# Kernel optimization log

Hardware: AMD Instinct MI355X
Metric: run time of the kernel (lower is better)

The kernel has to match this reference:

```python
import jax, jax.numpy as jnp
import numpy as np

H = 8
D_MODEL = 512
D_K = D_MODEL // H
NEG = -1e9


def setup_inputs() -> dict:
    key = jax.random.key(0)
    ks = jax.random.split(key, 11)
    B, S = 2, 2048
    scale = 1.0 / np.sqrt(D_MODEL)
    inp = {
        'query': jax.random.normal(ks[0], (B, S, D_MODEL), dtype=jnp.float32),
        'key': jax.random.normal(ks[1], (B, S, D_MODEL), dtype=jnp.float32),
        'value': jax.random.normal(ks[2], (B, S, D_MODEL), dtype=jnp.float32),
        'Wq': jax.random.normal(ks[3], (D_MODEL, D_MODEL), dtype=jnp.float32) * scale,
        'bq': jnp.zeros((D_MODEL,), dtype=jnp.float32),
        'Wk': jax.random.normal(ks[4], (D_MODEL, D_MODEL), dtype=jnp.float32) * scale,
        'bk': jnp.zeros((D_MODEL,), dtype=jnp.float32),
        'Wv': jax.random.normal(ks[5], (D_MODEL, D_MODEL), dtype=jnp.float32) * scale,
        'bv': jnp.zeros((D_MODEL,), dtype=jnp.float32),
        'Wo': jax.random.normal(ks[6], (D_MODEL, D_MODEL), dtype=jnp.float32) * scale,
        'bo': jnp.zeros((D_MODEL,), dtype=jnp.float32),
    }
    return inp


def reference(query, key, value, Wq, bq, Wk, bk, Wv, bv, Wo, bo):
    B, S, _ = query.shape
    # QKV projections (nn.Linear: x @ W.T + b), split into heads -> [B, H, S, D_K]
    def proj(x, W, b):
        return (x @ W.T + b).reshape(B, S, H, D_K).transpose(0, 2, 1, 3)

    q = proj(query, Wq, bq)
    k = proj(key, Wk, bk)
    v = proj(value, Wv, bv)

    scores = jnp.einsum('bhqd,bhkd->bhqk', q, k) / jnp.sqrt(jnp.float32(D_K))
    # diagonal mask (mask=True): token cannot attend to itself
    diag = jnp.eye(S, dtype=bool)
    scores = jnp.where(diag, NEG, scores)

    p_attn = jax.nn.softmax(scores, axis=-1)  # [B, H, S, S]
    x = jnp.einsum('bhqk,bhkd->bhqd', p_attn, v)
    x = x.transpose(0, 2, 1, 3).reshape(B, S, H * D_K)
    return x @ Wo.T + bo
```

## Files before the change

kernel.cpp:

```cpp
#include <hip/hip_runtime.h>
#include <hip/hip_bf16.h>
#include <hip/hip_fp16.h>
#include <math.h>

#define NUM_H 8
#define DK    64
#define DM    512
#define SEQ   2048
#define NB    2
#define MROWS (NB*SEQ)
#define NZ    4

typedef unsigned short u16;
typedef unsigned int   u32;
typedef __attribute__((ext_vector_type(8))) __bf16 bf16x8;
typedef __attribute__((ext_vector_type(4))) short  s16x4;
typedef __attribute__((ext_vector_type(4))) float  f32x4;

__device__ __forceinline__ u16 f2bf(float v) {
    union { __bf16 h; u16 u; } x; x.h = (__bf16)v; return x.u;
}
__device__ __forceinline__ u16 f2h(float v) {
    union { _Float16 h; u16 u; } x; x.h = (_Float16)v; return x.u;
}
__device__ __forceinline__ bf16x8 ld_bf8(const u16* p) {
    union { uint4 u; bf16x8 v; } t;
    t.u = *(const uint4*)p;
    return t.v;
}
__device__ __forceinline__ uint4 pack8bf(const float* f) {
    uint4 o;
    o.x = (u32)f2bf(f[0]) | ((u32)f2bf(f[1]) << 16);
    o.y = (u32)f2bf(f[2]) | ((u32)f2bf(f[3]) << 16);
    o.z = (u32)f2bf(f[4]) | ((u32)f2bf(f[5]) << 16);
    o.w = (u32)f2bf(f[6]) | ((u32)f2bf(f[7]) << 16);
    return o;
}
__device__ __forceinline__ float fexp2(float x) {
#if defined(__has_builtin) && __has_builtin(__builtin_amdgcn_exp2f)
    return __builtin_amdgcn_exp2f(x);
#else
    return exp2f(x);
#endif
}

__device__ __forceinline__ f32x4 mfma16bf(s16x4 a, s16x4 b, f32x4 c) {
#if defined(__has_builtin) && __has_builtin(__builtin_amdgcn_mfma_f32_16x16x16bf16_1k)
    return __builtin_amdgcn_mfma_f32_16x16x16bf16_1k(a, b, c, 0, 0, 0);
#else
    asm("v_mfma_f32_16x16x16_bf16 %0, %1, %2, %0" : "+v"(c) : "v"(a), "v"(b));
    return c;
#endif
}

__global__ __launch_bounds__(256) void convW(
    const float* __restrict__ Wq, const float* __restrict__ Wk,
    const float* __restrict__ Wv, const float* __restrict__ Wo,
    u16* __restrict__ Wscr)
{
    const int z = blockIdx.y;
    const float* src = (z == 0) ? Wq : (z == 1) ? Wk : (z == 2) ? Wv : Wo;
    u16* dst = Wscr + (size_t)z * 262144;
    int i = (blockIdx.x * 256 + threadIdx.x) * 8;
    float4 a = *(const float4*)(src + i);
    float4 b = *(const float4*)(src + i + 4);
    float f[8] = {a.x, a.y, a.z, a.w, b.x, b.y, b.z, b.w};
    *(uint4*)&dst[i] = pack8bf(f);
}

#define MODE_QK 0
#define MODE_VT 1
#define MODE_FIN 2

template<int MODE>
__device__ __forceinline__ void gemm_core(
    const void* __restrict__ Xv, const u16* __restrict__ Wb,
    const float* __restrict__ bias, const float* __restrict__ ClP,
    void* __restrict__ outv,
    u16* As, u16* Bs, int row0, int col0)
{
    const int tid = threadIdx.x;
    const int lane = tid & 63, w = tid >> 6;
    const int ln15 = lane & 15, quad = lane >> 4;
    const int wm = (w >> 1) * 32, wn = (w & 1) * 32;

    int cb0 = 0, cs0 = 0, cb1 = 0, cs1 = 0;
    if (MODE == MODE_FIN) {
        int m0 = row0 + (tid >> 3), m1 = m0 + 32;
        cb0 = (m0 >> 11) * NUM_H; cs0 = m0 & (SEQ - 1);
        cb1 = (m1 >> 11) * NUM_H; cs1 = m1 & (SEQ - 1);
    }

    f32x4 acc[2][2];
#pragma unroll
    for (int mt = 0; mt < 2; ++mt)
#pragma unroll
        for (int nt = 0; nt < 2; ++nt) acc[mt][nt] = (f32x4){0.f, 0.f, 0.f, 0.f};

    for (int kt = 0; kt < DM; kt += 64) {
        __syncthreads();
        if (MODE == MODE_FIN) {
            const int h = kt >> 6;
            float l0 = ClP[(cb0 + h) * SEQ + cs0] + ClP[32768 + (cb0 + h) * SEQ + cs0]
                     + ClP[65536 + (cb0 + h) * SEQ + cs0] + ClP[98304 + (cb0 + h) * SEQ + cs0];
            float l1 = ClP[(cb1 + h) * SEQ + cs1] + ClP[32768 + (cb1 + h) * SEQ + cs1]
                     + ClP[65536 + (cb1 + h) * SEQ + cs1] + ClP[98304 + (cb1 + h) * SEQ + cs1];
            float scr[2] = {64.f / l0, 64.f / l1};
#pragma unroll
            for (int g = 0; g < 2; ++g) {
                int r = g * 32 + (tid >> 3);
                int c = (tid & 7) * 8;
                const u16* pp = (const u16*)Xv + (size_t)(row0 + r) * DM + kt + c;
                union { uint4 u; __half2 h2[4]; } u0, u1, u2, u3;
                u0.u = *(const uint4*)pp;
                u1.u = *(const uint4*)(pp + 2097152);
                u2.u = *(const uint4*)(pp + 2 * 2097152);
                u3.u = *(const uint4*)(pp + 3 * 2097152);
                float f[8];
                float sc = scr[g];
#pragma unroll
                for (int j = 0; j < 4; ++j) {
                    __half2 s2 = __hadd2(__hadd2(u0.h2[j], u1.h2[j]),
                                         __hadd2(u2.h2[j], u3.h2[j]));
                    float2 fl = __half22float2(s2);
                    f[2 * j]     = fl.x * sc;
                    f[2 * j + 1] = fl.y * sc;
                }
                *(uint4*)&As[r * 72 + c] = pack8bf(f);
            }
        } else {
#pragma unroll
            for (int g = 0; g < 2; ++g) {
                int idx = g * 2048 + tid * 8;
                int r = idx >> 6, c = idx & 63;
                const float* xp = (const float*)Xv + (size_t)(row0 + r) * DM + kt + c;
                float4 a = *(const float4*)xp;
                float4 b2 = *(const float4*)(xp + 4);
                float f[8] = {a.x, a.y, a.z, a.w, b2.x, b2.y, b2.z, b2.w};
                *(uint4*)&As[r * 72 + c] = pack8bf(f);
            }
        }
#pragma unroll
        for (int g = 0; g < 2; ++g) {
            int idx = g * 2048 + tid * 8;
            int r = idx >> 6, c = idx & 63;
            *(uint4*)&Bs[r * 72 + c] =
                *(const uint4*)(Wb + (size_t)(col0 + r) * DM + kt + c);
        }
        __syncthreads();

#pragma unroll
        for (int ks = 0; ks < 2; ++ks) {
            bf16x8 af[2], bfr[2];
#pragma unroll
            for (int mt = 0; mt < 2; ++mt)
                af[mt] = ld_bf8(&As[(wm + mt * 16 + ln15) * 72 + ks * 32 + quad * 8]);
#pragma unroll
            for (int nt = 0; nt < 2; ++nt)
                bfr[nt] = ld_bf8(&Bs[(wn + nt * 16 + ln15) * 72 + ks * 32 + quad * 8]);
#pragma unroll
            for (int mt = 0; mt < 2; ++mt)
#pragma unroll
                for (int nt = 0; nt < 2; ++nt)
                    acc[mt][nt] = __builtin_amdgcn_mfma_f32_16x16x32_bf16(
                        af[mt], bfr[nt], acc[mt][nt], 0, 0, 0);
        }
    }

    float bc[2];
#pragma unroll
    for (int nt = 0; nt < 2; ++nt) bc[nt] = bias[col0 + wn + nt * 16 + ln15];
    const int h = col0 >> 6;

    if (MODE == MODE_FIN) {
        float* outF = (float*)outv;
#pragma unroll
        for (int mt = 0; mt < 2; ++mt)
#pragma unroll
            for (int r = 0; r < 4; ++r) {
                int m = row0 + wm + mt * 16 + quad * 4 + r;
#pragma unroll
                for (int nt = 0; nt < 2; ++nt)
                    outF[(size_t)m * DM + col0 + wn + nt * 16 + ln15] = acc[mt][nt][r] + bc[nt];
            }
    } else if (MODE == MODE_QK) {
        u16* outB = (u16*)outv;
#pragma unroll
        for (int mt = 0; mt < 2; ++mt)
#pragma unroll
            for (int r = 0; r < 4; ++r) {
                int m = row0 + wm + mt * 16 + quad * 4 + r;
                int b = m >> 11, s2 = m & (SEQ - 1);
#pragma unroll
                for (int nt = 0; nt < 2; ++nt) {
                    int dk = wn + nt * 16 + ln15;
                    outB[((size_t)((b * NUM_H + h) * SEQ + s2)) * DK + dk] =
                        f2bf(acc[mt][nt][r] + bc[nt]);
                }
            }
    } else {
        u16* outB = (u16*)outv;
        __syncthreads();
#pragma unroll
        for (int mt = 0; mt < 2; ++mt)
#pragma unroll
            for (int nt = 0; nt < 2; ++nt) {
                int dk = wn + nt * 16 + ln15;
#pragma unroll
                for (int r = 0; r < 4; ++r) {
                    int sl = wm + mt * 16 + quad * 4 + r;
                    As[dk * 72 + sl] = f2bf(acc[mt][nt][r] + bc[nt]);
                }
            }
        __syncthreads();
        int dk = tid >> 2, ch = (tid & 3) * 16;
        int b = row0 >> 11, s0 = row0 & (SEQ - 1);
        size_t base = ((size_t)((b * NUM_H + h) * DK + dk)) * SEQ + s0 + ch;
        *(uint4*)&outB[base]     = *(const uint4*)&As[dk * 72 + ch];
        *(uint4*)&outB[base + 8] = *(const uint4*)&As[dk * 72 + ch + 8];
    }
}

__global__ __launch_bounds__(256) void qkv_mfma(
    const float* __restrict__ xq, const float* __restrict__ xk, const float* __restrict__ xv,
    const u16* __restrict__ Wscr,
    const float* __restrict__ b0, const float* __restrict__ b1, const float* __restrict__ b2,
    u16* __restrict__ oQ, u16* __restrict__ oK, u16* __restrict__ oVt)
{
    __shared__ u16 As[64 * 72];
    __shared__ u16 Bs[64 * 72];
    const int row0 = blockIdx.x * 64, col0 = blockIdx.y * 64;
    const int z = blockIdx.z;
    const u16* W = Wscr + (size_t)z * 262144;
    if (z == 2)
        gemm_core<MODE_VT>(xv, W, b2, nullptr, oVt, As, Bs, row0, col0);
    else if (z == 0)
        gemm_core<MODE_QK>(xq, W, b0, nullptr, oQ, As, Bs, row0, col0);
    else
        gemm_core<MODE_QK>(xk, W, b1, nullptr, oK, As, Bs, row0, col0);
}

__global__ __launch_bounds__(256) void final_mfma(
    const u16* __restrict__ Pd, const u16* __restrict__ Wbf,
    const float* __restrict__ Cl, const float* __restrict__ bias,
    float* __restrict__ out)
{
    __shared__ u16 As[64 * 72];
    __shared__ u16 Bs[64 * 72];
    gemm_core<MODE_FIN>(Pd, Wbf, bias, Cl, out, As, Bs,
                        blockIdx.x * 64, blockIdx.y * 64);
}

#define LSTR 72
#define SCL2  0.18033688f
#define BIA2 -5.7708020f
__global__ __launch_bounds__(256) void attn_mfma(
    const u16* __restrict__ Qg, const u16* __restrict__ Kg,
    const u16* __restrict__ Vtg, u16* __restrict__ Pd, float* __restrict__ Cl)
{
    __shared__ u16 Klds[64 * LSTR];
    __shared__ u16 Vtlds[64 * LSTR];

    const int tid = threadIdx.x;
    const int lane = tid & 63;
    const int w = tid >> 6;
    const int ln15 = lane & 15;
    const int quad = lane >> 4;
    const int bh = blockIdx.y;
    const int b = bh >> 3, h = bh & 7;
    const int qb = blockIdx.x * 64;
    const int z = blockIdx.z;
    const int k0 = z * (SEQ / NZ), k1 = k0 + SEQ / NZ;

    const u16* Qp = Qg + (size_t)bh * SEQ * DK;
    const u16* Kp = Kg + (size_t)bh * SEQ * DK;
    const u16* Vp = Vtg + (size_t)bh * DK * SEQ;

    const int myq = w * 16 + ln15;
    const int qrow = qb + myq;
    const bf16x8 qa0 = ld_bf8(&Qp[(size_t)qrow * DK + quad * 8]);
    const bf16x8 qa1 = ld_bf8(&Qp[(size_t)qrow * DK + 32 + quad * 8]);

    const bool mrow = (quad == (ln15 >> 2));
    const int  mr   = ln15 & 3;

    const s16x4 onesb = (s16x4){(short)0x3F80, (short)0x3F80,
                                (short)0x3F80, (short)0x3F80};

    f32x4 O[4];
    f32x4 Lacc = (f32x4){0.f, 0.f, 0.f, 0.f};
#pragma unroll
    for (int nt = 0; nt < 4; ++nt) O[nt] = (f32x4){0.f, 0.f, 0.f, 0.f};

    const int sr = tid >> 3;
    const int scl = (tid & 7) * 8;
    const u16* kp0 = &Kp[(size_t)sr * DK + scl];
    const u16* kp1 = &Kp[(size_t)(sr + 32) * DK + scl];
    const u16* vp0 = &Vp[(size_t)sr * SEQ + scl];
    const u16* vp1 = &Vp[(size_t)(sr + 32) * SEQ + scl];

    uint4 kreg0 = *(const uint4*)&kp0[(size_t)k0 * DK];
    uint4 kreg1 = *(const uint4*)&kp1[(size_t)k0 * DK];
    uint4 vreg0 = *(const uint4*)&vp0[k0];
    uint4 vreg1 = *(const uint4*)&vp1[k0];

    for (int kt = k0; kt < k1; kt += 64) {
        *(uint4*)&Klds[sr * LSTR + scl]         = kreg0;
        *(uint4*)&Klds[(sr + 32) * LSTR + scl]  = kreg1;
        *(uint4*)&Vtlds[sr * LSTR + scl]        = vreg0;
        *(uint4*)&Vtlds[(sr + 32) * LSTR + scl] = vreg1;
        __syncthreads();

        if (kt + 64 < k1) {
            kreg0 = *(const uint4*)&kp0[(size_t)(kt + 64) * DK];
            kreg1 = *(const uint4*)&kp1[(size_t)(kt + 64) * DK];
            vreg0 = *(const uint4*)&vp0[kt + 64];
            vreg1 = *(const uint4*)&vp1[kt + 64];
        }

        const bool diagt = (kt == qb);
        s16x4 pa[4];
#pragma unroll
        for (int nt2 = 0; nt2 < 4; ++nt2) {
            bf16x8 kb0 = ld_bf8(&Klds[(nt2 * 16 + ln15) * LSTR + quad * 8]);
            bf16x8 kb1 = ld_bf8(&Klds[(nt2 * 16 + ln15) * LSTR + 32 + quad * 8]);
            f32x4 zacc = (f32x4){0.f, 0.f, 0.f, 0.f};
            zacc = __builtin_amdgcn_mfma_f32_16x16x32_bf16(kb0, qa0, zacc, 0, 0, 0);
            zacc = __builtin_amdgcn_mfma_f32_16x16x32_bf16(kb1, qa1, zacc, 0, 0, 0);
            union { u16 u[4]; s16x4 v; } pk;
#pragma unroll
            for (int r = 0; r < 4; ++r)
                pk.u[r] = f2bf(fexp2(fmaf(zacc[r], SCL2, BIA2)));
            if (diagt && nt2 == w) {
#pragma unroll
                for (int r = 0; r < 4; ++r)
                    if (mrow && r == mr) pk.u[r] = 0;
            }
            pa[nt2] = pk.v;
        }

        const u16* vb_base = &Vtlds[ln15 * LSTR + quad * 4];
        __builtin_amdgcn_s_setprio(1);
#pragma unroll
        for (int nt2 = 0; nt2 < 4; ++nt2)
            Lacc = mfma16bf(pa[nt2], onesb, Lacc);
#pragma unroll
        for (int nt = 0; nt < 4; ++nt) {
#pragma unroll
            for (int nt2 = 0; nt2 < 4; ++nt2) {
                s16x4 vb = *(const s16x4*)&vb_base[nt * 16 * LSTR + nt2 * 16];
                O[nt] = mfma16bf(pa[nt2], vb, O[nt]);
            }
        }
        __builtin_amdgcn_s_setprio(0);
        __syncthreads();
    }

    if (ln15 == 0) {
#pragma unroll
        for (int r = 0; r < 4; ++r)
            Cl[(size_t)z * 32768 + bh * SEQ + qb + w * 16 + quad * 4 + r] = Lacc[r];
    }

#pragma unroll
    for (int r = 0; r < 4; ++r) {
        int s = qb + w * 16 + quad * 4 + r;
        size_t base = (size_t)z * 2097152 + ((size_t)(b * SEQ + s)) * DM + h * DK;
#pragma unroll
        for (int nt = 0; nt < 4; ++nt)
            Pd[base + nt * 16 + ln15] = f2h(O[nt][r] * 0.015625f);
    }
}

extern "C" void kernel_launch(void* const* d_in, const int* in_sizes, int n_in,
                              void* d_out, int out_size, void* d_ws, size_t ws_size,
                              hipStream_t stream) {
    const float* q  = (const float*)d_in[0];
    const float* k  = (const float*)d_in[1];
    const float* v  = (const float*)d_in[2];
    const float* Wq = (const float*)d_in[3];
    const float* bq = (const float*)d_in[4];
    const float* Wk = (const float*)d_in[5];
    const float* bk = (const float*)d_in[6];
    const float* Wv = (const float*)d_in[7];
    const float* bv = (const float*)d_in[8];
    const float* Wo = (const float*)d_in[9];
    const float* bo = (const float*)d_in[10];
    float* out = (float*)d_out;

    const size_t TSZ = (size_t)MROWS * DM;
    u16* Qb   = (u16*)d_ws;
    u16* Kb   = Qb + TSZ;
    u16* Vtb  = Qb + 2 * TSZ;
    float* Cl = (float*)(Qb + 3 * TSZ);
    u16* Wscr = (u16*)(Cl + 131072);
    u16* Pd   = Wscr + 4 * 262144;

    dim3 blk(256);
    hipLaunchKernelGGL(convW, dim3(128, 4), blk, 0, stream, Wq, Wk, Wv, Wo, Wscr);
    dim3 gq(MROWS / 64, DM / 64, 3);
    hipLaunchKernelGGL(qkv_mfma, gq, blk, 0, stream,
                       q, k, v, Wscr, bq, bk, bv, Qb, Kb, Vtb);
    dim3 ga(SEQ / 64, NB * NUM_H, NZ);
    hipLaunchKernelGGL(attn_mfma, ga, blk, 0, stream, Qb, Kb, Vtb, Pd, Cl);
    dim3 gf(MROWS / 64, DM / 64);
    hipLaunchKernelGGL(final_mfma, gf, blk, 0, stream, Pd, Wscr + 3 * 262144, Cl, bo, out);
}
```

Baseline: 149.9 us.

## Pre-convert activations to bf16 and register-prefetch next GEMM tile

The weight-conversion kernel is extended to also convert the three fp32 input activations to bf16 in a workspace buffer, so the QKV GEMM loads half as many bytes per tile. The GEMM core is restructured to prefetch the next K-tile into registers while MFMAs run on the current shared tile. The final GEMM precomputes all per-head softmax normalizers up front instead of per iteration. This adds an extra full pass over the inputs (read fp32, write bf16, reread) plus register pressure from eight prefetched uint4 in FIN mode.

```diff
diff --git a/kernel.cpp b/kernel.cpp
--- a/kernel.cpp
+++ b/kernel.cpp
@@ -53,14 +53,24 @@
 #endif
 }
 
-__global__ __launch_bounds__(256) void convW(
+__global__ __launch_bounds__(256) void convAll(
     const float* __restrict__ Wq, const float* __restrict__ Wk,
     const float* __restrict__ Wv, const float* __restrict__ Wo,
-    u16* __restrict__ Wscr)
+    const float* __restrict__ xq, const float* __restrict__ xk,
+    const float* __restrict__ xv,
+    u16* __restrict__ Wscr, u16* __restrict__ Xb)
 {
     const int z = blockIdx.y;
-    const float* src = (z == 0) ? Wq : (z == 1) ? Wk : (z == 2) ? Wv : Wo;
-    u16* dst = Wscr + (size_t)z * 262144;
+    const float* src;
+    u16* dst;
+    if (z < 4) {
+        if (blockIdx.x >= 128) return;
+        src = (z == 0) ? Wq : (z == 1) ? Wk : (z == 2) ? Wv : Wo;
+        dst = Wscr + (size_t)z * 262144;
+    } else {
+        src = (z == 4) ? xq : (z == 5) ? xk : xv;
+        dst = Xb + (size_t)(z - 4) * 2097152;
+    }
     int i = (blockIdx.x * 256 + threadIdx.x) * 8;
     float4 a = *(const float4*)(src + i);
     float4 b = *(const float4*)(src + i + 4);
@@ -74,7 +84,7 @@
 
 template<int MODE>
 __device__ __forceinline__ void gemm_core(
-    const void* __restrict__ Xv, const u16* __restrict__ Wb,
+    const u16* __restrict__ Xb, const u16* __restrict__ Wb,
     const float* __restrict__ bias, const float* __restrict__ ClP,
     void* __restrict__ outv,
     u16* As, u16* Bs, int row0, int col0)
@@ -83,12 +93,30 @@
     const int lane = tid & 63, w = tid >> 6;
     const int ln15 = lane & 15, quad = lane >> 4;
     const int wm = (w >> 1) * 32, wn = (w & 1) * 32;
-
-    int cb0 = 0, cs0 = 0, cb1 = 0, cs1 = 0;
+    const int sr = tid >> 3;
+    const int scl = (tid & 7) * 8;
+
+    const u16* a0p = Xb + (size_t)(row0 + sr) * DM + scl;
+    const u16* a1p = Xb + (size_t)(row0 + 32 + sr) * DM + scl;
+    const u16* b0p = Wb + (size_t)(col0 + sr) * DM + scl;
+    const u16* b1p = Wb + (size_t)(col0 + 32 + sr) * DM + scl;
+
+    float scr0[8], scr1[8];
     if (MODE == MODE_FIN) {
-        int m0 = row0 + (tid >> 3), m1 = m0 + 32;
-        cb0 = (m0 >> 11) * NUM_H; cs0 = m0 & (SEQ - 1);
-        cb1 = (m1 >> 11) * NUM_H; cs1 = m1 & (SEQ - 1);
+        int m0 = row0 + sr, m1 = m0 + 32;
+        int cb0 = (m0 >> 11) * NUM_H, cs0 = m0 & (SEQ - 1);
+        int cb1 = (m1 >> 11) * NUM_H, cs1 = m1 & (SEQ - 1);
+#pragma unroll
+        for (int hh = 0; hh < 8; ++hh) {
+            float l0 = 0.f, l1 = 0.f;
+#pragma unroll
+            for (int zz = 0; zz < NZ; ++zz) {
+                l0 += ClP[zz * 32768 + (cb0 + hh) * SEQ + cs0];
+                l1 += ClP[zz * 32768 + (cb1 + hh) * SEQ + cs1];
+            }
+            scr0[hh] = 64.f / l0;
+            scr1[hh] = 64.f / l1;
+        }
     }
 
     f32x4 acc[2][2];
@@ -97,57 +125,75 @@
 #pragma unroll
         for (int nt = 0; nt < 2; ++nt) acc[mt][nt] = (f32x4){0.f, 0.f, 0.f, 0.f};
 
+    uint4 ra0, ra1, rb0, rb1;
+    uint4 rp00, rp01, rp02, rp03, rp10, rp11, rp12, rp13;
+    if (MODE == MODE_FIN) {
+        rp00 = *(const uint4*)(a0p);
+        rp01 = *(const uint4*)(a0p + 2097152);
+        rp02 = *(const uint4*)(a0p + 2 * 2097152);
+        rp03 = *(const uint4*)(a0p + 3 * 2097152);
+        rp10 = *(const uint4*)(a1p);
+        rp11 = *(const uint4*)(a1p + 2097152);
+        rp12 = *(const uint4*)(a1p + 2 * 2097152);
+        rp13 = *(const uint4*)(a1p + 3 * 2097152);
+    } else {
+        ra0 = *(const uint4*)a0p;
+        ra1 = *(const uint4*)a1p;
+    }
+    rb0 = *(const uint4*)b0p;
+    rb1 = *(const uint4*)b1p;
+
+#pragma unroll
     for (int kt = 0; kt < DM; kt += 64) {
-        __syncthreads();
+        const int h = kt >> 6;
         if (MODE == MODE_FIN) {
-            const int h = kt >> 6;
-            float l0 = ClP[(cb0 + h) * SEQ + cs0] + ClP[32768 + (cb0 + h) * SEQ + cs0]
-                     + ClP[65536 + (cb0 + h) * SEQ + cs0] + ClP[98304 + (cb0 + h) * SEQ + cs0];
-            float l1 = ClP[(cb1 + h) * SEQ + cs1] + ClP[32768 + (cb1 + h) * SEQ + cs1]
-                     + ClP[65536 + (cb1 + h) * SEQ + cs1] + ClP[98304 + (cb1 + h) * SEQ + cs1];
-            float scr[2] = {64.f / l0, 64.f / l1};
-#pragma unroll
-            for (int g = 0; g < 2; ++g) {
-                int r = g * 32 + (tid >> 3);
-                int c = (tid & 7) * 8;
-                const u16* pp = (const u16*)Xv + (size_t)(row0 + r) * DM + kt + c;
-                union { uint4 u; __half2 h2[4]; } u0, u1, u2, u3;
-                u0.u = *(const uint4*)pp;
-                u1.u = *(const uint4*)(pp + 2097152);
-                u2.u = *(const uint4*)(pp + 2 * 2097152);
-                u3.u = *(const uint4*)(pp + 3 * 2097152);
-                float f[8];
-                float sc = scr[g];
-#pragma unroll
-                for (int j = 0; j < 4; ++j) {
-                    __half2 s2 = __hadd2(__hadd2(u0.h2[j], u1.h2[j]),
-                                         __hadd2(u2.h2[j], u3.h2[j]));
-                    float2 fl = __half22float2(s2);
-                    f[2 * j]     = fl.x * sc;
-                    f[2 * j + 1] = fl.y * sc;
-                }
-                *(uint4*)&As[r * 72 + c] = pack8bf(f);
-            }
+            union { uint4 u; __half2 h2[4]; } u0, u1, u2, u3;
+            float f[8];
+            u0.u = rp00; u1.u = rp01; u2.u = rp02; u3.u = rp03;
+#pragma unroll
+            for (int j = 0; j < 4; ++j) {
+                __half2 s2 = __hadd2(__hadd2(u0.h2[j], u1.h2[j]),
+                                     __hadd2(u2.h2[j], u3.h2[j]));
+                float2 fl = __half22float2(s2);
+                f[2 * j]     = fl.x * scr0[h];
+                f[2 * j + 1] = fl.y * scr0[h];
+            }
+            *(uint4*)&As[sr * 72 + scl] = pack8bf(f);
+            u0.u = rp10; u1.u = rp11; u2.u = rp12; u3.u = rp13;
+#pragma unroll
+            for (int j = 0; j < 4; ++j) {
+                __half2 s2 = __hadd2(__hadd2(u0.h2[j], u1.h2[j]),
+                                     __hadd2(u2.h2[j], u3.h2[j]));
+                float2 fl = __half22float2(s2);
+                f[2 * j]     = fl.x * scr1[h];
+                f[2 * j + 1] = fl.y * scr1[h];
+            }
+            *(uint4*)&As[(sr + 32) * 72 + scl] = pack8bf(f);
         } else {
-#pragma unroll
-            for (int g = 0; g < 2; ++g) {
-                int idx = g * 2048 + tid * 8;
-                int r = idx >> 6, c = idx & 63;
-                const float* xp = (const float*)Xv + (size_t)(row0 + r) * DM + kt + c;
-                float4 a = *(const float4*)xp;
-                float4 b2 = *(const float4*)(xp + 4);
-                float f[8] = {a.x, a.y, a.z, a.w, b2.x, b2.y, b2.z, b2.w};
-                *(uint4*)&As[r * 72 + c] = pack8bf(f);
-            }
-        }
-#pragma unroll
-        for (int g = 0; g < 2; ++g) {
-            int idx = g * 2048 + tid * 8;
-            int r = idx >> 6, c = idx & 63;
-            *(uint4*)&Bs[r * 72 + c] =
-                *(const uint4*)(Wb + (size_t)(col0 + r) * DM + kt + c);
-        }
-        __syncthreads();
+            *(uint4*)&As[sr * 72 + scl]        = ra0;
+            *(uint4*)&As[(sr + 32) * 72 + scl] = ra1;
+        }
+        *(uint4*)&Bs[sr * 72 + scl]        = rb0;
+        *(uint4*)&Bs[(sr + 32) * 72 + scl] = rb1;
+        __syncthreads();
+
+        if (kt + 64 < DM) {
+            if (MODE == MODE_FIN) {
+                rp00 = *(const uint4*)(a0p + kt + 64);
+                rp01 = *(const uint4*)(a0p + kt + 64 + 2097152);
+                rp02 = *(const uint4*)(a0p + kt + 64 + 2 * 2097152);
+                rp03 = *(const uint4*)(a0p + kt + 64 + 3 * 2097152);
+                rp10 = *(const uint4*)(a1p + kt + 64);
+                rp11 = *(const uint4*)(a1p + kt + 64 + 2097152);
+                rp12 = *(const uint4*)(a1p + kt + 64 + 2 * 2097152);
+                rp13 = *(const uint4*)(a1p + kt + 64 + 3 * 2097152);
+            } else {
+                ra0 = *(const uint4*)(a0p + kt + 64);
+                ra1 = *(const uint4*)(a1p + kt + 64);
+            }
+            rb0 = *(const uint4*)(b0p + kt + 64);
+            rb1 = *(const uint4*)(b1p + kt + 64);
+        }
 
 #pragma unroll
         for (int ks = 0; ks < 2; ++ks) {
@@ -165,6 +211,7 @@
                     acc[mt][nt] = __builtin_amdgcn_mfma_f32_16x16x32_bf16(
                         af[mt], bfr[nt], acc[mt][nt], 0, 0, 0);
         }
+        __syncthreads();
     }
 
     float bc[2];
@@ -222,22 +269,23 @@
 }
 
 __global__ __launch_bounds__(256) void qkv_mfma(
-    const float* __restrict__ xq, const float* __restrict__ xk, const float* __restrict__ xv,
-    const u16* __restrict__ Wscr,
-    const float* __restrict__ b0, const float* __restrict__ b1, const float* __restrict__ b2,
+    const u16* __restrict__ Xb, const u16* __restrict__ Wscr,
+    const float* __restrict__ b0, const float* __restrict__ b1,
+    const float* __restrict__ b2,
     u16* __restrict__ oQ, u16* __restrict__ oK, u16* __restrict__ oVt)
 {
     __shared__ u16 As[64 * 72];
     __shared__ u16 Bs[64 * 72];
     const int row0 = blockIdx.x * 64, col0 = blockIdx.y * 64;
     const int z = blockIdx.z;
+    const u16* X = Xb + (size_t)z * 2097152;
     const u16* W = Wscr + (size_t)z * 262144;
     if (z == 2)
-        gemm_core<MODE_VT>(xv, W, b2, nullptr, oVt, As, Bs, row0, col0);
+        gemm_core<MODE_VT>(X, W, b2, nullptr, oVt, As, Bs, row0, col0);
     else if (z == 0)
-        gemm_core<MODE_QK>(xq, W, b0, nullptr, oQ, As, Bs, row0, col0);
+        gemm_core<MODE_QK>(X, W, b0, nullptr, oQ, As, Bs, row0, col0);
     else
-        gemm_core<MODE_QK>(xk, W, b1, nullptr, oK, As, Bs, row0, col0);
+        gemm_core<MODE_QK>(X, W, b1, nullptr, oK, As, Bs, row0, col0);
 }
 
 __global__ __launch_bounds__(256) void final_mfma(
@@ -395,12 +443,14 @@
     float* Cl = (float*)(Qb + 3 * TSZ);
     u16* Wscr = (u16*)(Cl + 131072);
     u16* Pd   = Wscr + 4 * 262144;
+    u16* Xb   = Pd + (size_t)NZ * TSZ;
 
     dim3 blk(256);
-    hipLaunchKernelGGL(convW, dim3(128, 4), blk, 0, stream, Wq, Wk, Wv, Wo, Wscr);
+    hipLaunchKernelGGL(convAll, dim3(1024, 7), blk, 0, stream,
+                       Wq, Wk, Wv, Wo, q, k, v, Wscr, Xb);
     dim3 gq(MROWS / 64, DM / 64, 3);
     hipLaunchKernelGGL(qkv_mfma, gq, blk, 0, stream,
-                       q, k, v, Wscr, bq, bk, bv, Qb, Kb, Vtb);
+                       Xb, Wscr, bq, bk, bv, Qb, Kb, Vtb);
     dim3 ga(SEQ / 64, NB * NUM_H, NZ);
     hipLaunchKernelGGL(attn_mfma, ga, blk, 0, stream, Qb, Kb, Vtb, Pd, Cl);
     dim3 gf(MROWS / 64, DM / 64);
```

Measured after the change: 154.4 us. +3.0%, slower.

## Process 128 query rows per attention block to reuse K/V tiles

Applied to the files above, without the earlier changes.

Each attention workgroup now handles 128 query rows instead of 64, with every wave computing two 16-row query subtiles against each K/V tile staged in LDS. This halves the number of K/V global loads and LDS staging passes per query and gives each wave more independent MFMA chains to interleave. The grid is reordered so the key-split index varies fastest, and the launch bounds ask for four blocks per CU. The cost is more accumulator and P registers per wave, which could cause spills or lower occupancy, plus half as many blocks in the grid.

```diff
diff --git a/kernel.cpp b/kernel.cpp
--- a/kernel.cpp
+++ b/kernel.cpp
@@ -254,7 +254,7 @@
 #define LSTR 72
 #define SCL2  0.18033688f
 #define BIA2 -5.7708020f
-__global__ __launch_bounds__(256) void attn_mfma(
+__global__ __launch_bounds__(256, 4) void attn_mfma(
     const u16* __restrict__ Qg, const u16* __restrict__ Kg,
     const u16* __restrict__ Vtg, u16* __restrict__ Pd, float* __restrict__ Cl)
 {
@@ -268,29 +268,37 @@
     const int quad = lane >> 4;
     const int bh = blockIdx.y;
     const int b = bh >> 3, h = bh & 7;
-    const int qb = blockIdx.x * 64;
-    const int z = blockIdx.z;
+    const int qb = blockIdx.z * 128;
+    const int z = blockIdx.x;
     const int k0 = z * (SEQ / NZ), k1 = k0 + SEQ / NZ;
 
     const u16* Qp = Qg + (size_t)bh * SEQ * DK;
     const u16* Kp = Kg + (size_t)bh * SEQ * DK;
     const u16* Vp = Vtg + (size_t)bh * DK * SEQ;
 
-    const int myq = w * 16 + ln15;
-    const int qrow = qb + myq;
-    const bf16x8 qa0 = ld_bf8(&Qp[(size_t)qrow * DK + quad * 8]);
-    const bf16x8 qa1 = ld_bf8(&Qp[(size_t)qrow * DK + 32 + quad * 8]);
+    const int myq0 = w * 32 + ln15;
+    bf16x8 qa[2][2];
+    qa[0][0] = ld_bf8(&Qp[(size_t)(qb + myq0) * DK + quad * 8]);
+    qa[0][1] = ld_bf8(&Qp[(size_t)(qb + myq0) * DK + 32 + quad * 8]);
+    qa[1][0] = ld_bf8(&Qp[(size_t)(qb + myq0 + 16) * DK + quad * 8]);
+    qa[1][1] = ld_bf8(&Qp[(size_t)(qb + myq0 + 16) * DK + 32 + quad * 8]);
 
     const bool mrow = (quad == (ln15 >> 2));
     const int  mr   = ln15 & 3;
+    const int  diag_kt = qb + (w >> 1) * 64;
+    const int  nt2d = (w & 1) * 2;
 
     const s16x4 onesb = (s16x4){(short)0x3F80, (short)0x3F80,
                                 (short)0x3F80, (short)0x3F80};
 
-    f32x4 O[4];
-    f32x4 Lacc = (f32x4){0.f, 0.f, 0.f, 0.f};
-#pragma unroll
-    for (int nt = 0; nt < 4; ++nt) O[nt] = (f32x4){0.f, 0.f, 0.f, 0.f};
+    f32x4 O[2][4];
+    f32x4 Lacc[2];
+#pragma unroll
+    for (int s = 0; s < 2; ++s) {
+        Lacc[s] = (f32x4){0.f, 0.f, 0.f, 0.f};
+#pragma unroll
+        for (int nt = 0; nt < 4; ++nt) O[s][nt] = (f32x4){0.f, 0.f, 0.f, 0.f};
+    }
 
     const int sr = tid >> 3;
     const int scl = (tid & 7) * 8;
@@ -318,38 +326,44 @@
             vreg1 = *(const uint4*)&vp1[kt + 64];
         }
 
-        const bool diagt = (kt == qb);
-        s16x4 pa[4];
+        const bool diagt = (kt == diag_kt);
+        s16x4 pa[2][4];
 #pragma unroll
         for (int nt2 = 0; nt2 < 4; ++nt2) {
             bf16x8 kb0 = ld_bf8(&Klds[(nt2 * 16 + ln15) * LSTR + quad * 8]);
             bf16x8 kb1 = ld_bf8(&Klds[(nt2 * 16 + ln15) * LSTR + 32 + quad * 8]);
-            f32x4 zacc = (f32x4){0.f, 0.f, 0.f, 0.f};
-            zacc = __builtin_amdgcn_mfma_f32_16x16x32_bf16(kb0, qa0, zacc, 0, 0, 0);
-            zacc = __builtin_amdgcn_mfma_f32_16x16x32_bf16(kb1, qa1, zacc, 0, 0, 0);
-            union { u16 u[4]; s16x4 v; } pk;
-#pragma unroll
-            for (int r = 0; r < 4; ++r)
-                pk.u[r] = f2bf(fexp2(fmaf(zacc[r], SCL2, BIA2)));
-            if (diagt && nt2 == w) {
+#pragma unroll
+            for (int s = 0; s < 2; ++s) {
+                f32x4 zacc = (f32x4){0.f, 0.f, 0.f, 0.f};
+                zacc = __builtin_amdgcn_mfma_f32_16x16x32_bf16(kb0, qa[s][0], zacc, 0, 0, 0);
+                zacc = __builtin_amdgcn_mfma_f32_16x16x32_bf16(kb1, qa[s][1], zacc, 0, 0, 0);
+                union { u16 u[4]; s16x4 v; } pk;
 #pragma unroll
                 for (int r = 0; r < 4; ++r)
-                    if (mrow && r == mr) pk.u[r] = 0;
-            }
-            pa[nt2] = pk.v;
+                    pk.u[r] = f2bf(fexp2(fmaf(zacc[r], SCL2, BIA2)));
+                if (diagt && nt2 == nt2d + s) {
+#pragma unroll
+                    for (int r = 0; r < 4; ++r)
+                        if (mrow && r == mr) pk.u[r] = 0;
+                }
+                pa[s][nt2] = pk.v;
+            }
         }
 
         const u16* vb_base = &Vtlds[ln15 * LSTR + quad * 4];
         __builtin_amdgcn_s_setprio(1);
 #pragma unroll
-        for (int nt2 = 0; nt2 < 4; ++nt2)
-            Lacc = mfma16bf(pa[nt2], onesb, Lacc);
+        for (int nt2 = 0; nt2 < 4; ++nt2) {
+            Lacc[0] = mfma16bf(pa[0][nt2], onesb, Lacc[0]);
+            Lacc[1] = mfma16bf(pa[1][nt2], onesb, Lacc[1]);
+        }
 #pragma unroll
         for (int nt = 0; nt < 4; ++nt) {
 #pragma unroll
             for (int nt2 = 0; nt2 < 4; ++nt2) {
                 s16x4 vb = *(const s16x4*)&vb_base[nt * 16 * LSTR + nt2 * 16];
-                O[nt] = mfma16bf(pa[nt2], vb, O[nt]);
+                O[0][nt] = mfma16bf(pa[0][nt2], vb, O[0][nt]);
+                O[1][nt] = mfma16bf(pa[1][nt2], vb, O[1][nt]);
             }
         }
         __builtin_amdgcn_s_setprio(0);
@@ -358,18 +372,23 @@
 
     if (ln15 == 0) {
 #pragma unroll
-        for (int r = 0; r < 4; ++r)
-            Cl[(size_t)z * 32768 + bh * SEQ + qb + w * 16 + quad * 4 + r] = Lacc[r];
-    }
-
-#pragma unroll
-    for (int r = 0; r < 4; ++r) {
-        int s = qb + w * 16 + quad * 4 + r;
-        size_t base = (size_t)z * 2097152 + ((size_t)(b * SEQ + s)) * DM + h * DK;
-#pragma unroll
-        for (int nt = 0; nt < 4; ++nt)
-            Pd[base + nt * 16 + ln15] = f2h(O[nt][r] * 0.015625f);
-    }
+        for (int s = 0; s < 2; ++s)
+#pragma unroll
+            for (int r = 0; r < 4; ++r)
+                Cl[(size_t)z * 32768 + bh * SEQ + qb + w * 32 + s * 16 + quad * 4 + r]
+                    = Lacc[s][r];
+    }
+
+#pragma unroll
+    for (int s = 0; s < 2; ++s)
+#pragma unroll
+        for (int r = 0; r < 4; ++r) {
+            int sq = qb + w * 32 + s * 16 + quad * 4 + r;
+            size_t base = (size_t)z * 2097152 + ((size_t)(b * SEQ + sq)) * DM + h * DK;
+#pragma unroll
+            for (int nt = 0; nt < 4; ++nt)
+                Pd[base + nt * 16 + ln15] = f2h(O[s][nt][r] * 0.015625f);
+        }
 }
 
 extern "C" void kernel_launch(void* const* d_in, const int* in_sizes, int n_in,
@@ -401,7 +420,7 @@
     dim3 gq(MROWS / 64, DM / 64, 3);
     hipLaunchKernelGGL(qkv_mfma, gq, blk, 0, stream,
                        q, k, v, Wscr, bq, bk, bv, Qb, Kb, Vtb);
-    dim3 ga(SEQ / 64, NB * NUM_H, NZ);
+    dim3 ga(NZ, NB * NUM_H, SEQ / 128);
     hipLaunchKernelGGL(attn_mfma, ga, blk, 0, stream, Qb, Kb, Vtb, Pd, Cl);
     dim3 gf(MROWS / 64, DM / 64);
     hipLaunchKernelGGL(final_mfma, gf, blk, 0, stream, Pd, Wscr + 3 * 262144, Cl, bo, out);
```

New measurement: 146.9 us. -2.0%, faster.

## Rewrite attention inner loop with 32x32x16 MFMA and 128-query blocks

Applied to the files above, without the earlier changes.

The attention kernel switches from 16x16 MFMA tiles to 32x32x16 bf16 MFMA. Each block now covers 128 queries (32 per wave), so every K/V tile loaded into LDS is reused across twice as many queries and the number of blocks is halved. The P fragment is rearranged between lane halves with v_permlane32_swap instead of being fed through a separate path. Row sums are accumulated in scalar registers rather than with extra MFMAs against a ones vector, and the grid order puts the key-split index fastest. The larger accumulators raise register pressure, which launch_bounds(256,4) tries to contain, and the diagonal-mask index mapping is more intricate.

```diff
diff --git a/kernel.cpp b/kernel.cpp
--- a/kernel.cpp
+++ b/kernel.cpp
@@ -13,9 +13,9 @@
 
 typedef unsigned short u16;
 typedef unsigned int   u32;
-typedef __attribute__((ext_vector_type(8))) __bf16 bf16x8;
-typedef __attribute__((ext_vector_type(4))) short  s16x4;
-typedef __attribute__((ext_vector_type(4))) float  f32x4;
+typedef __attribute__((ext_vector_type(8)))  __bf16 bf16x8;
+typedef __attribute__((ext_vector_type(4)))  float  f32x4;
+typedef __attribute__((ext_vector_type(16))) float  f32x16;
 
 __device__ __forceinline__ u16 f2bf(float v) {
     union { __bf16 h; u16 u; } x; x.h = (__bf16)v; return x.u;
@@ -43,14 +43,16 @@
     return exp2f(x);
 #endif
 }
-
-__device__ __forceinline__ f32x4 mfma16bf(s16x4 a, s16x4 b, f32x4 c) {
-#if defined(__has_builtin) && __has_builtin(__builtin_amdgcn_mfma_f32_16x16x16bf16_1k)
-    return __builtin_amdgcn_mfma_f32_16x16x16bf16_1k(a, b, c, 0, 0, 0);
-#else
-    asm("v_mfma_f32_16x16x16_bf16 %0, %1, %2, %0" : "+v"(c) : "v"(a), "v"(b));
-    return c;
-#endif
+__device__ __forceinline__ u32 pk2(float lo, float hi) {
+    return (u32)f2bf(lo) | ((u32)f2bf(hi) << 16);
+}
+__device__ __forceinline__ bf16x8 frag4(u32 w0, u32 w1, u32 w2, u32 w3) {
+    union { u32 u[4]; bf16x8 v; } t;
+    t.u[0] = w0; t.u[1] = w1; t.u[2] = w2; t.u[3] = w3;
+    return t.v;
+}
+__device__ __forceinline__ f32x16 mfma32(bf16x8 a, bf16x8 b, f32x16 c) {
+    return __builtin_amdgcn_mfma_f32_32x32x16_bf16(a, b, c, 0, 0, 0);
 }
 
 __global__ __launch_bounds__(256) void convW(
@@ -254,7 +256,7 @@
 #define LSTR 72
 #define SCL2  0.18033688f
 #define BIA2 -5.7708020f
-__global__ __launch_bounds__(256) void attn_mfma(
+__global__ __launch_bounds__(256, 4) void attn_mfma(
     const u16* __restrict__ Qg, const u16* __restrict__ Kg,
     const u16* __restrict__ Vtg, u16* __restrict__ Pd, float* __restrict__ Cl)
 {
@@ -264,33 +266,32 @@
     const int tid = threadIdx.x;
     const int lane = tid & 63;
     const int w = tid >> 6;
-    const int ln15 = lane & 15;
-    const int quad = lane >> 4;
+    const int col = lane & 31;
+    const int hi  = lane >> 5;
+    const int hi8 = hi * 8;
     const int bh = blockIdx.y;
     const int b = bh >> 3, h = bh & 7;
-    const int qb = blockIdx.x * 64;
-    const int z = blockIdx.z;
+    const int qb = blockIdx.z * 128;
+    const int z = blockIdx.x;
     const int k0 = z * (SEQ / NZ), k1 = k0 + SEQ / NZ;
 
     const u16* Qp = Qg + (size_t)bh * SEQ * DK;
     const u16* Kp = Kg + (size_t)bh * SEQ * DK;
     const u16* Vp = Vtg + (size_t)bh * DK * SEQ;
 
-    const int myq = w * 16 + ln15;
-    const int qrow = qb + myq;
-    const bf16x8 qa0 = ld_bf8(&Qp[(size_t)qrow * DK + quad * 8]);
-    const bf16x8 qa1 = ld_bf8(&Qp[(size_t)qrow * DK + 32 + quad * 8]);
-
-    const bool mrow = (quad == (ln15 >> 2));
-    const int  mr   = ln15 & 3;
-
-    const s16x4 onesb = (s16x4){(short)0x3F80, (short)0x3F80,
-                                (short)0x3F80, (short)0x3F80};
-
-    f32x4 O[4];
-    f32x4 Lacc = (f32x4){0.f, 0.f, 0.f, 0.f};
-#pragma unroll
-    for (int nt = 0; nt < 4; ++nt) O[nt] = (f32x4){0.f, 0.f, 0.f, 0.f};
+    const int myq = qb + w * 32 + col;
+    bf16x8 qf[4];
+#pragma unroll
+    for (int dkb = 0; dkb < 4; ++dkb)
+        qf[dkb] = ld_bf8(&Qp[(size_t)myq * DK + dkb * 16 + hi8]);
+
+    const int diag_kt = qb + (w >> 1) * 64;
+    const int vtarget = col - 4 * hi;
+
+    f32x16 O0 = {0.f, 0.f, 0.f, 0.f, 0.f, 0.f, 0.f, 0.f,
+                 0.f, 0.f, 0.f, 0.f, 0.f, 0.f, 0.f, 0.f};
+    f32x16 O1 = O0;
+    float lsum = 0.f;
 
     const int sr = tid >> 3;
     const int scl = (tid & 7) * 8;
@@ -318,57 +319,59 @@
             vreg1 = *(const uint4*)&vp1[kt + 64];
         }
 
-        const bool diagt = (kt == qb);
-        s16x4 pa[4];
-#pragma unroll
-        for (int nt2 = 0; nt2 < 4; ++nt2) {
-            bf16x8 kb0 = ld_bf8(&Klds[(nt2 * 16 + ln15) * LSTR + quad * 8]);
-            bf16x8 kb1 = ld_bf8(&Klds[(nt2 * 16 + ln15) * LSTR + 32 + quad * 8]);
-            f32x4 zacc = (f32x4){0.f, 0.f, 0.f, 0.f};
-            zacc = __builtin_amdgcn_mfma_f32_16x16x32_bf16(kb0, qa0, zacc, 0, 0, 0);
-            zacc = __builtin_amdgcn_mfma_f32_16x16x32_bf16(kb1, qa1, zacc, 0, 0, 0);
-            union { u16 u[4]; s16x4 v; } pk;
-#pragma unroll
-            for (int r = 0; r < 4; ++r)
-                pk.u[r] = f2bf(fexp2(fmaf(zacc[r], SCL2, BIA2)));
-            if (diagt && nt2 == w) {
-#pragma unroll
-                for (int r = 0; r < 4; ++r)
-                    if (mrow && r == mr) pk.u[r] = 0;
-            }
-            pa[nt2] = pk.v;
-        }
-
-        const u16* vb_base = &Vtlds[ln15 * LSTR + quad * 4];
+        const bool diagt = (kt == diag_kt);
         __builtin_amdgcn_s_setprio(1);
 #pragma unroll
-        for (int nt2 = 0; nt2 < 4; ++nt2)
-            Lacc = mfma16bf(pa[nt2], onesb, Lacc);
-#pragma unroll
-        for (int nt = 0; nt < 4; ++nt) {
-#pragma unroll
-            for (int nt2 = 0; nt2 < 4; ++nt2) {
-                s16x4 vb = *(const s16x4*)&vb_base[nt * 16 * LSTR + nt2 * 16];
-                O[nt] = mfma16bf(pa[nt2], vb, O[nt]);
+        for (int kb32 = 0; kb32 < 2; ++kb32) {
+            f32x16 z16 = {0.f, 0.f, 0.f, 0.f, 0.f, 0.f, 0.f, 0.f,
+                          0.f, 0.f, 0.f, 0.f, 0.f, 0.f, 0.f, 0.f};
+#pragma unroll
+            for (int dkb = 0; dkb < 4; ++dkb) {
+                bf16x8 kf = ld_bf8(&Klds[(kb32 * 32 + col) * LSTR + dkb * 16 + hi8]);
+                z16 = mfma32(kf, qf[dkb], z16);
+            }
+            const bool dm = diagt && (kb32 == (w & 1));
+#pragma unroll
+            for (int c = 0; c < 2; ++c) {
+                float e[8];
+#pragma unroll
+                for (int i = 0; i < 8; ++i) {
+                    const int r = c * 8 + i;
+                    float ee = fexp2(fmaf(z16[r], SCL2, BIA2));
+                    const int crow0 = (r & 3) + 8 * (r >> 2);
+                    if (dm && vtarget == crow0) ee = 0.f;
+                    lsum += ee;
+                    e[i] = ee;
+                }
+                u32 a0 = pk2(e[0], e[1]);
+                u32 a1 = pk2(e[2], e[3]);
+                u32 a2 = pk2(e[4], e[5]);
+                u32 a3 = pk2(e[6], e[7]);
+                asm("v_permlane32_swap_b32 %0, %1" : "+v"(a0), "+v"(a2));
+                asm("v_permlane32_swap_b32 %0, %1" : "+v"(a1), "+v"(a3));
+                bf16x8 paf = frag4(a0, a1, a2, a3);
+                const int kb16 = kb32 * 2 + c;
+                bf16x8 vf0 = ld_bf8(&Vtlds[col * LSTR + kb16 * 16 + hi8]);
+                bf16x8 vf1 = ld_bf8(&Vtlds[(32 + col) * LSTR + kb16 * 16 + hi8]);
+                O0 = mfma32(paf, vf0, O0);
+                O1 = mfma32(paf, vf1, O1);
             }
         }
         __builtin_amdgcn_s_setprio(0);
         __syncthreads();
     }
 
-    if (ln15 == 0) {
-#pragma unroll
-        for (int r = 0; r < 4; ++r)
-            Cl[(size_t)z * 32768 + bh * SEQ + qb + w * 16 + quad * 4 + r] = Lacc[r];
-    }
-
-#pragma unroll
-    for (int r = 0; r < 4; ++r) {
-        int s = qb + w * 16 + quad * 4 + r;
-        size_t base = (size_t)z * 2097152 + ((size_t)(b * SEQ + s)) * DM + h * DK;
-#pragma unroll
-        for (int nt = 0; nt < 4; ++nt)
-            Pd[base + nt * 16 + ln15] = f2h(O[nt][r] * 0.015625f);
+    float lt = lsum + __shfl_xor(lsum, 32);
+    if (lane < 32)
+        Cl[(size_t)z * 32768 + bh * SEQ + qb + w * 32 + col] = lt;
+
+#pragma unroll
+    for (int reg = 0; reg < 16; ++reg) {
+        const int crow = (reg & 3) + 8 * (reg >> 2) + 4 * hi;
+        const int sq = qb + w * 32 + crow;
+        size_t base = (size_t)z * 2097152 + ((size_t)(b * SEQ + sq)) * DM + h * DK;
+        Pd[base + col]      = f2h(O0[reg] * 0.015625f);
+        Pd[base + 32 + col] = f2h(O1[reg] * 0.015625f);
     }
 }
 
@@ -401,7 +404,7 @@
     dim3 gq(MROWS / 64, DM / 64, 3);
     hipLaunchKernelGGL(qkv_mfma, gq, blk, 0, stream,
                        q, k, v, Wscr, bq, bk, bv, Qb, Kb, Vtb);
-    dim3 ga(SEQ / 64, NB * NUM_H, NZ);
+    dim3 ga(NZ, NB * NUM_H, SEQ / 128);
     hipLaunchKernelGGL(attn_mfma, ga, blk, 0, stream, Qb, Kb, Vtb, Pd, Cl);
     dim3 gf(MROWS / 64, DM / 64);
     hipLaunchKernelGGL(final_mfma, gf, blk, 0, stream, Pd, Wscr + 3 * 262144, Cl, bo, out);
```

Result: no change. 149.8 us (-0.0%).
